# Performance work log

Measured on AMD Instinct MI355X. Metric: run time of the kernel, lower is better.

The kernel has to match this reference:

```python
import jax, jax.numpy as jnp
import numpy as np
import math

DIM = 1024
HEAD = 16


def setup_inputs() -> dict:
    key = jax.random.key(0)
    k1, k2, k3, k4, k5 = jax.random.split(key, 5)
    scale = 1.0 / math.sqrt(DIM)
    return {
        "x": jax.random.normal(k1, (2, 2048, DIM), dtype=jnp.float32),
        "W_kqv": jax.random.uniform(k2, (3 * DIM, DIM), minval=-scale, maxval=scale, dtype=jnp.float32),
        "b_kqv": jax.random.uniform(k3, (3 * DIM,), minval=-scale, maxval=scale, dtype=jnp.float32),
        "W_out": jax.random.uniform(k4, (DIM, DIM), minval=-scale, maxval=scale, dtype=jnp.float32),
        "b_out": jax.random.uniform(k5, (DIM,), minval=-scale, maxval=scale, dtype=jnp.float32),
    }


def reference(x, W_kqv, b_kqv, W_out, b_out):
    b, s, h = x.shape
    head = HEAD
    d = h // head
    # fused QKV projection (torch Linear: x @ W.T + b)
    kqv = jnp.einsum("bsh,oh->bso", x, W_kqv) + b_kqv  # [b, s, 3h]
    q, k, v = jnp.split(kqv, 3, axis=-1)
    # [b, s, h] -> [b, head, s, d]
    q = q.reshape(b, s, head, d).transpose(0, 2, 1, 3)
    k = k.reshape(b, s, head, d).transpose(0, 2, 1, 3)
    v = v.reshape(b, s, head, d).transpose(0, 2, 1, 3)
    scores = jnp.einsum("bnqd,bnkd->bnqk", q, k) / jnp.sqrt(jnp.float32(d))
    attn = jax.nn.softmax(scores, axis=-1)
    ctx = jnp.einsum("bnqk,bnkd->bnqd", attn, v)  # [b, head, s, d]
    ctx = ctx.transpose(0, 2, 1, 3).reshape(b, s, h)
    return jnp.einsum("bsh,oh->bso", ctx, W_out) + b_out
```

## Files before the change

kernel.cpp:

```cpp
#include <hip/hip_runtime.h>
#include <hip/hip_bf16.h>

#define DIM   1024
#define NHEAD 16
#define HD    64
#define SEQ   2048
#define BATCH 2
#define QKV3  3072

using short8 = __attribute__((ext_vector_type(8))) short;
using f32x4  = __attribute__((ext_vector_type(4))) float;

__device__ inline short f2bf(float f) {
    union { float f; unsigned u; } x; x.f = f;
    const unsigned r = (x.u + 0x7FFFu + ((x.u >> 16) & 1u)) >> 16;
    return (short)r;
}
__device__ inline unsigned pkbf(float a, float b) {
    union { __hip_bfloat162 h; unsigned u; } cv;
    cv.h = __float22bfloat162_rn(make_float2(a, b));
    return cv.u;
}

__device__ __forceinline__ void g2l16(const void* gptr, void* ldsbase) {
    __builtin_amdgcn_global_load_lds(
        (const __attribute__((address_space(1))) unsigned int*)(unsigned long long)gptr,
        (__attribute__((address_space(3))) unsigned int*)(unsigned int)(unsigned long long)ldsbase,
        16, 0, 0);
}

__global__ __launch_bounds__(256)
void conv_bf16(const float* __restrict__ x, const float* __restrict__ wk,
               const float* __restrict__ wo,
               unsigned short* __restrict__ xb, unsigned short* __restrict__ wkb,
               unsigned short* __restrict__ wob)
{
    const int bid = blockIdx.x;
    const float* src; unsigned short* dst; size_t base;
    if (bid < 1024)      { src = x;  dst = xb;  base = (size_t)bid * 4096; }
    else if (bid < 1792) { src = wk; dst = wkb; base = (size_t)(bid - 1024) * 4096; }
    else                 { src = wo; dst = wob; base = (size_t)(bid - 1792) * 4096; }
    const size_t off = base + threadIdx.x * 16;
    const float4 f0 = *(const float4*)(src + off + 0);
    const float4 f1 = *(const float4*)(src + off + 4);
    const float4 f2 = *(const float4*)(src + off + 8);
    const float4 f3 = *(const float4*)(src + off + 12);
    uint4 o0, o1;
    o0.x = pkbf(f0.x, f0.y); o0.y = pkbf(f0.z, f0.w);
    o0.z = pkbf(f1.x, f1.y); o0.w = pkbf(f1.z, f1.w);
    o1.x = pkbf(f2.x, f2.y); o1.y = pkbf(f2.z, f2.w);
    o1.z = pkbf(f3.x, f3.y); o1.w = pkbf(f3.z, f3.w);
    *(uint4*)(dst + off + 0) = o0;
    *(uint4*)(dst + off + 8) = o1;
}

__global__ __launch_bounds__(256)
void gemm_qkv(const unsigned short* __restrict__ A, const unsigned short* __restrict__ B,
              const float* __restrict__ bias,
              unsigned short* __restrict__ qbf, unsigned short* __restrict__ kbf,
              unsigned short* __restrict__ vtbf)
{
    constexpr int BK = 32, NIT = DIM / BK;
    const int K = DIM;
    __shared__ short As[2][128 * BK];
    __shared__ short Bs[2][128 * BK];

    const int tid  = threadIdx.x;
    const int lane = tid & 63;
    const int wave = tid >> 6;
    const int quad = lane >> 4;
    const int ln   = lane & 15;
    const int wm   = (wave & 1) * 64;
    const int wn   = (wave >> 1) * 64;

    const int bid = blockIdx.x;
    const int xcd = bid & 7;
    const int t   = bid >> 3;
    const int m0  = (xcd * 4 + (t & 3)) * 128;
    const int n0  = (t >> 2) * 128;

    int srow[2], sg[2];
#pragma unroll
    for (int i = 0; i < 2; ++i) {
        const int c  = wave * 128 + i * 64 + lane;
        srow[i] = c >> 2;
        sg[i]   = (c & 3) ^ ((srow[i] >> 1) & 3);
    }

    f32x4 acc[4][4];
#pragma unroll
    for (int i = 0; i < 4; ++i)
#pragma unroll
        for (int j = 0; j < 4; ++j) acc[i][j] = (f32x4){0.f, 0.f, 0.f, 0.f};

#pragma unroll
    for (int i = 0; i < 2; ++i) {
        const int cb = wave * 128 + i * 64;
        g2l16(A + (size_t)(m0 + srow[i]) * K + sg[i] * 8, &As[0][cb * 8]);
        g2l16(B + (size_t)(n0 + srow[i]) * K + sg[i] * 8, &Bs[0][cb * 8]);
    }
    __syncthreads();

    for (int kt = 0; kt < NIT; ++kt) {
        const int p = kt & 1;
        if (kt + 1 < NIT) {
            const int kn = (kt + 1) * BK;
#pragma unroll
            for (int i = 0; i < 2; ++i) {
                const int cb = wave * 128 + i * 64;
                g2l16(A + (size_t)(m0 + srow[i]) * K + kn + sg[i] * 8, &As[1 - p][cb * 8]);
                g2l16(B + (size_t)(n0 + srow[i]) * K + kn + sg[i] * 8, &Bs[1 - p][cb * 8]);
            }
        }

        short8 a[4], b[4];
#pragma unroll
        for (int i = 0; i < 4; ++i) {
            const int row = wm + i * 16 + ln;
            const int ch  = quad ^ ((row >> 1) & 3);
            a[i] = *(const short8*)&As[p][row * BK + ch * 8];
        }
#pragma unroll
        for (int j = 0; j < 4; ++j) {
            const int row = wn + j * 16 + ln;
            const int ch  = quad ^ ((row >> 1) & 3);
            b[j] = *(const short8*)&Bs[p][row * BK + ch * 8];
        }
#pragma unroll
        for (int i = 0; i < 4; ++i)
#pragma unroll
            for (int j = 0; j < 4; ++j)
                acc[i][j] = __builtin_amdgcn_mfma_f32_16x16x32_bf16(
                    a[i], b[j], acc[i][j], 0, 0, 0);
        __syncthreads();
    }

#pragma unroll
    for (int j = 0; j < 4; ++j) {
        const int col = n0 + wn + j * 16 + ln;
        const int sel = col >> 10;
        const int c   = col & 1023;
        const int hh  = c >> 6;
        const int dd  = c & 63;
        const float bv = bias[col];
        if (sel < 2) {
            unsigned short* dst = (sel == 0) ? qbf : kbf;
            const float qs = (sel == 0) ? 0.18033688f : 1.0f;
#pragma unroll
            for (int i = 0; i < 4; ++i)
#pragma unroll
                for (int r2 = 0; r2 < 4; ++r2) {
                    const int row = m0 + wm + i * 16 + quad * 4 + r2;
                    const int bb = row >> 11, ss = row & 2047;
                    dst[((size_t)(bb * NHEAD + hh) * SEQ + ss) * HD + dd] =
                        (unsigned short)f2bf((acc[i][j][r2] + bv) * qs);
                }
        } else {
            const int row0 = m0 + wm + quad * 4;
            const int bb = row0 >> 11;
            const size_t vbase = ((size_t)(bb * NHEAD + hh) * HD + dd) * SEQ;
#pragma unroll
            for (int i = 0; i < 4; ++i) {
                const int ss0 = (row0 & 2047) + i * 16;
                uint2 pk;
                pk.x = pkbf(acc[i][j][0] + bv, acc[i][j][1] + bv);
                pk.y = pkbf(acc[i][j][2] + bv, acc[i][j][3] + bv);
                *(uint2*)&vtbf[vbase + ss0] = pk;
            }
        }
    }
}

__global__ __launch_bounds__(512)
void attn_flash_mfma(const unsigned short* __restrict__ qbf,
                     const unsigned short* __restrict__ kbf,
                     const unsigned short* __restrict__ vtbf,
                     unsigned short* __restrict__ ctxbf)
{
    __shared__ short Ks[2][2][64 * 64];
    __shared__ short Vt[2][2][64 * 64];

    const int tid  = threadIdx.x;
    const int lane = tid & 63;
    const int wave = tid >> 6;
    const int hf   = wave >> 2;
    const int w4   = wave & 3;
    const int quad = lane >> 4;
    const int ln   = lane & 15;

    const int bid = blockIdx.x;
    const int bh  = bid & 31;
    const int qt  = bid >> 5;
    const int q0  = qt * 128;
    const int b   = bh >> 4;
    const int h   = bh & 15;

    const size_t sbase = (size_t)bh * SEQ * HD;
    const size_t vbase = (size_t)bh * HD * SEQ;
    const int kv0 = hf * (SEQ / 2);

    const int tloc = tid & 255;
    int srw[2], scg[2];
#pragma unroll
    for (int it = 0; it < 2; ++it) {
        const int ch = tloc + it * 256;
        srw[it] = ch >> 3;
        scg[it] = (ch & 7) ^ (srw[it] & 7);
    }

    short8 qf[2][2];
#pragma unroll
    for (int sm = 0; sm < 2; ++sm)
#pragma unroll
        for (int kc = 0; kc < 2; ++kc)
            qf[sm][kc] = *(const short8*)&qbf[sbase +
                (size_t)(q0 + w4 * 32 + sm * 16 + ln) * HD + kc * 32 + quad * 8];

#pragma unroll
    for (int it = 0; it < 2; ++it) {
        const int cb = tloc + it * 256;
        g2l16(kbf + sbase + (size_t)(kv0 + srw[it]) * HD + scg[it] * 8,
              &Ks[0][hf][cb * 8]);
        g2l16(vtbf + vbase + (size_t)srw[it] * SEQ + kv0 + scg[it] * 8,
              &Vt[0][hf][cb * 8]);
    }
    __syncthreads();

    f32x4 O[2][4];
#pragma unroll
    for (int sm = 0; sm < 2; ++sm)
#pragma unroll
        for (int dj = 0; dj < 4; ++dj) O[sm][dj] = (f32x4){0.f, 0.f, 0.f, 0.f};
    f32x4 lacc[2];
    lacc[0] = (f32x4){0.f, 0.f, 0.f, 0.f};
    lacc[1] = (f32x4){0.f, 0.f, 0.f, 0.f};

    short8 vone;
#pragma unroll
    for (int t = 0; t < 8; ++t) vone[t] = (short)0x3F80;

    constexpr int NIT = (SEQ / 2) / 64;
    for (int kt = 0; kt < NIT; ++kt) {
        const int p = kt & 1;
        if (kt + 1 < NIT) {
            const int k0n = kv0 + (kt + 1) * 64;
#pragma unroll
            for (int it = 0; it < 2; ++it) {
                const int cb = tloc + it * 256;
                g2l16(kbf + sbase + (size_t)(k0n + srw[it]) * HD + scg[it] * 8,
                      &Ks[1 - p][hf][cb * 8]);
                g2l16(vtbf + vbase + (size_t)srw[it] * SEQ + k0n + scg[it] * 8,
                      &Vt[1 - p][hf][cb * 8]);
            }
        }

        f32x4 st[2][4];
        __builtin_amdgcn_s_setprio(1);
#pragma unroll
        for (int j = 0; j < 4; ++j) {
            const int row = j * 16 + ln;
            const int c0 = quad ^ (row & 7);
            const int c1 = (4 + quad) ^ (row & 7);
            const short8 kf0 = *(const short8*)&Ks[p][hf][row * 64 + c0 * 8];
            const short8 kf1 = *(const short8*)&Ks[p][hf][row * 64 + c1 * 8];
#pragma unroll
            for (int sm = 0; sm < 2; ++sm) {
                f32x4 tt = __builtin_amdgcn_mfma_f32_16x16x32_bf16(
                    kf0, qf[sm][0], (f32x4){0.f, 0.f, 0.f, 0.f}, 0, 0, 0);
                st[sm][j] = __builtin_amdgcn_mfma_f32_16x16x32_bf16(
                    kf1, qf[sm][1], tt, 0, 0, 0);
            }
        }
        __builtin_amdgcn_s_setprio(0);

        short8 pf[2][2];
#pragma unroll
        for (int sm = 0; sm < 2; ++sm) {
            unsigned lo[4], hi[4];
#pragma unroll
            for (int j = 0; j < 4; ++j) {
                const float e0 = __builtin_amdgcn_exp2f(st[sm][j][0]);
                const float e1 = __builtin_amdgcn_exp2f(st[sm][j][1]);
                const float e2 = __builtin_amdgcn_exp2f(st[sm][j][2]);
                const float e3 = __builtin_amdgcn_exp2f(st[sm][j][3]);
                lo[j] = pkbf(e0, e1);
                hi[j] = pkbf(e2, e3);
            }
#pragma unroll
            for (int kc = 0; kc < 2; ++kc) {
                auto sa = __builtin_amdgcn_permlane32_swap(lo[2 * kc], lo[2 * kc + 1], false, false);
                auto sb = __builtin_amdgcn_permlane32_swap(hi[2 * kc], hi[2 * kc + 1], false, false);
                auto ua = __builtin_amdgcn_permlane16_swap(sa[0], sa[1], false, false);
                auto ub = __builtin_amdgcn_permlane16_swap(sb[0], sb[1], false, false);
                union { unsigned u[4]; short8 s; } cv;
                cv.u[0] = ua[0];
                cv.u[1] = ub[0];
                cv.u[2] = ua[1];
                cv.u[3] = ub[1];
                pf[sm][kc] = cv.s;
            }
        }

        __builtin_amdgcn_s_setprio(1);
#pragma unroll
        for (int kc = 0; kc < 2; ++kc) {
            lacc[0] = __builtin_amdgcn_mfma_f32_16x16x32_bf16(pf[0][kc], vone, lacc[0], 0, 0, 0);
            lacc[1] = __builtin_amdgcn_mfma_f32_16x16x32_bf16(pf[1][kc], vone, lacc[1], 0, 0, 0);
#pragma unroll
            for (int dj = 0; dj < 4; ++dj) {
                const int row = dj * 16 + ln;
                const int cg  = (kc * 4 + quad) ^ (row & 7);
                const short8 vf = *(const short8*)&Vt[p][hf][row * 64 + cg * 8];
                O[0][dj] = __builtin_amdgcn_mfma_f32_16x16x32_bf16(pf[0][kc], vf, O[0][dj], 0, 0, 0);
                O[1][dj] = __builtin_amdgcn_mfma_f32_16x16x32_bf16(pf[1][kc], vf, O[1][dj], 0, 0, 0);
            }
        }
        __builtin_amdgcn_s_setprio(0);
        __syncthreads();
    }

    float* Of = (float*)&Ks[0][0][0];
    float* Lf = (float*)&Vt[0][0][0];
    if (hf == 0) {
#pragma unroll
        for (int sm = 0; sm < 2; ++sm) {
#pragma unroll
            for (int dj = 0; dj < 4; ++dj)
#pragma unroll
                for (int r2 = 0; r2 < 4; ++r2)
                    Of[(w4 * 32 + sm * 16 + quad * 4 + r2) * 64 + dj * 16 + ln] =
                        O[sm][dj][r2];
            if (ln == 0)
#pragma unroll
                for (int r2 = 0; r2 < 4; ++r2)
                    Lf[w4 * 32 + sm * 16 + quad * 4 + r2] = lacc[sm][r2];
        }
    }
    __syncthreads();
    if (hf == 1) {
#pragma unroll
        for (int sm = 0; sm < 2; ++sm)
#pragma unroll
            for (int r2 = 0; r2 < 4; ++r2) {
                const int rr = w4 * 32 + sm * 16 + quad * 4 + r2;
                const float inv = 1.0f / (lacc[sm][r2] + Lf[rr]);
                const int row = b * SEQ + q0 + rr;
#pragma unroll
                for (int dj = 0; dj < 4; ++dj) {
                    const float val = O[sm][dj][r2] + Of[rr * 64 + dj * 16 + ln];
                    ctxbf[(size_t)row * DIM + h * HD + dj * 16 + ln] =
                        (unsigned short)f2bf(val * inv);
                }
            }
    }
}

__global__ __launch_bounds__(256)
void gemm_out(const unsigned short* __restrict__ A, const unsigned short* __restrict__ B,
              const float* __restrict__ bias, float* __restrict__ C)
{
    constexpr int BK = 32, NIT = DIM / BK;
    const int K = DIM, N = DIM;
    __shared__ short As[2][128 * BK];
    __shared__ short Bs[2][64 * BK];

    const int tid  = threadIdx.x;
    const int lane = tid & 63;
    const int wave = tid >> 6;
    const int quad = lane >> 4;
    const int ln   = lane & 15;
    const int wm   = (wave & 1) * 64;
    const int wn   = (wave >> 1) * 32;

    const int bid = blockIdx.x;
    const int xcd = bid & 7;
    const int t   = bid >> 3;
    const int m0  = (xcd * 4 + (t & 3)) * 128;
    const int n0  = (t >> 2) * 64;

    int srow[2], sg[2];
#pragma unroll
    for (int i = 0; i < 2; ++i) {
        const int c  = wave * 128 + i * 64 + lane;
        srow[i] = c >> 2;
        sg[i]   = (c & 3) ^ ((srow[i] >> 1) & 3);
    }
    const int cB  = wave * 64 + lane;
    const int brow = cB >> 2;
    const int bg   = (cB & 3) ^ ((brow >> 1) & 3);

    f32x4 acc[4][2];
#pragma unroll
    for (int i = 0; i < 4; ++i)
#pragma unroll
        for (int j = 0; j < 2; ++j) acc[i][j] = (f32x4){0.f, 0.f, 0.f, 0.f};

#pragma unroll
    for (int i = 0; i < 2; ++i)
        g2l16(A + (size_t)(m0 + srow[i]) * K + sg[i] * 8,
              &As[0][(wave * 128 + i * 64) * 8]);
    g2l16(B + (size_t)(n0 + brow) * K + bg * 8, &Bs[0][(wave * 64) * 8]);
    __syncthreads();

    for (int kt = 0; kt < NIT; ++kt) {
        const int p = kt & 1;
        if (kt + 1 < NIT) {
            const int kn = (kt + 1) * BK;
#pragma unroll
            for (int i = 0; i < 2; ++i)
                g2l16(A + (size_t)(m0 + srow[i]) * K + kn + sg[i] * 8,
                      &As[1 - p][(wave * 128 + i * 64) * 8]);
            g2l16(B + (size_t)(n0 + brow) * K + kn + bg * 8, &Bs[1 - p][(wave * 64) * 8]);
        }

        short8 a[4], b[2];
#pragma unroll
        for (int i = 0; i < 4; ++i) {
            const int row = wm + i * 16 + ln;
            const int ch  = quad ^ ((row >> 1) & 3);
            a[i] = *(const short8*)&As[p][row * BK + ch * 8];
        }
#pragma unroll
        for (int j = 0; j < 2; ++j) {
            const int row = wn + j * 16 + ln;
            const int ch  = quad ^ ((row >> 1) & 3);
            b[j] = *(const short8*)&Bs[p][row * BK + ch * 8];
        }
#pragma unroll
        for (int i = 0; i < 4; ++i)
#pragma unroll
            for (int j = 0; j < 2; ++j)
                acc[i][j] = __builtin_amdgcn_mfma_f32_16x16x32_bf16(
                    a[i], b[j], acc[i][j], 0, 0, 0);
        __syncthreads();
    }

#pragma unroll
    for (int j = 0; j < 2; ++j) {
        const int col = n0 + wn + j * 16 + ln;
        const float bv = bias[col];
#pragma unroll
        for (int i = 0; i < 4; ++i)
#pragma unroll
            for (int r2 = 0; r2 < 4; ++r2) {
                const int row = m0 + wm + i * 16 + quad * 4 + r2;
                C[(size_t)row * N + col] = acc[i][j][r2] + bv;
            }
    }
}

extern "C" void kernel_launch(void* const* d_in, const int* in_sizes, int n_in,
                              void* d_out, int out_size, void* d_ws, size_t ws_size,
                              hipStream_t stream)
{
    const float* x     = (const float*)d_in[0];
    const float* W_kqv = (const float*)d_in[1];
    const float* b_kqv = (const float*)d_in[2];
    const float* W_out = (const float*)d_in[3];
    const float* b_out = (const float*)d_in[4];
    float* out = (float*)d_out;

    char* w = (char*)d_ws;
    unsigned short* qbf   = (unsigned short*)w;  w += (size_t)BATCH * NHEAD * SEQ * HD * 2;
    unsigned short* kbf   = (unsigned short*)w;  w += (size_t)BATCH * NHEAD * SEQ * HD * 2;
    unsigned short* vtbf  = (unsigned short*)w;  w += (size_t)BATCH * NHEAD * HD * SEQ * 2;
    unsigned short* ctxbf = (unsigned short*)w;  w += (size_t)BATCH * SEQ * DIM * 2;
    unsigned short* xb    = (unsigned short*)w;  w += (size_t)BATCH * SEQ * DIM * 2;
    unsigned short* wkb   = (unsigned short*)w;  w += (size_t)QKV3 * DIM * 2;
    unsigned short* wob   = (unsigned short*)w;

    dim3 blk(256);

    conv_bf16<<<dim3(2048), blk, 0, stream>>>(x, W_kqv, W_out, xb, wkb, wob);

    gemm_qkv<<<dim3(768), blk, 0, stream>>>(xb, wkb, b_kqv, qbf, kbf, vtbf);

    attn_flash_mfma<<<dim3(512), dim3(512), 0, stream>>>(qbf, kbf, vtbf, ctxbf);

    gemm_out<<<dim3(512), blk, 0, stream>>>(ctxbf, wob, b_out, out);
}
```

Measured before the change: 175.9 us.

## Triple-buffer GEMM LDS stages with one barrier per K-step

Both projection GEMMs (QKV and output) move from double to triple-buffered LDS. Prefetch runs two K-tiles ahead, and explicit vmcnt waits let the current tile's loads finish while the next tile's loads stay in flight. Each K iteration now has a single barrier instead of two, and the next prefetch is issued after the LDS reads complete so it overlaps the MFMAs. This uses more LDS, which may reduce occupancy, and it relies on hand-set waitcnt values matching the number of async loads each thread issues.

```diff
diff --git a/kernel.cpp b/kernel.cpp
--- a/kernel.cpp
+++ b/kernel.cpp
@@ -62,8 +62,8 @@
 {
     constexpr int BK = 32, NIT = DIM / BK;
     const int K = DIM;
-    __shared__ short As[2][128 * BK];
-    __shared__ short Bs[2][128 * BK];
+    __shared__ short As[3][128 * BK];
+    __shared__ short Bs[3][128 * BK];
 
     const int tid  = threadIdx.x;
     const int lane = tid & 63;
@@ -94,45 +94,59 @@
         for (int j = 0; j < 4; ++j) acc[i][j] = (f32x4){0.f, 0.f, 0.f, 0.f};
 
 #pragma unroll
-    for (int i = 0; i < 2; ++i) {
-        const int cb = wave * 128 + i * 64;
-        g2l16(A + (size_t)(m0 + srow[i]) * K + sg[i] * 8, &As[0][cb * 8]);
-        g2l16(B + (size_t)(n0 + srow[i]) * K + sg[i] * 8, &Bs[0][cb * 8]);
-    }
-    __syncthreads();
-
+    for (int t0 = 0; t0 < 2; ++t0) {
+        const int kn = t0 * BK;
+#pragma unroll
+        for (int i = 0; i < 2; ++i) {
+            const int cb = wave * 128 + i * 64;
+            g2l16(A + (size_t)(m0 + srow[i]) * K + kn + sg[i] * 8, &As[t0][cb * 8]);
+            g2l16(B + (size_t)(n0 + srow[i]) * K + kn + sg[i] * 8, &Bs[t0][cb * 8]);
+        }
+    }
+
+    int bufc = 0;
+    int bufn = 2;
     for (int kt = 0; kt < NIT; ++kt) {
-        const int p = kt & 1;
-        if (kt + 1 < NIT) {
-            const int kn = (kt + 1) * BK;
-#pragma unroll
-            for (int i = 0; i < 2; ++i) {
-                const int cb = wave * 128 + i * 64;
-                g2l16(A + (size_t)(m0 + srow[i]) * K + kn + sg[i] * 8, &As[1 - p][cb * 8]);
-                g2l16(B + (size_t)(n0 + srow[i]) * K + kn + sg[i] * 8, &Bs[1 - p][cb * 8]);
-            }
-        }
+        if (kt < NIT - 1) asm volatile("s_waitcnt vmcnt(4)" ::: "memory");
+        else              asm volatile("s_waitcnt vmcnt(0)" ::: "memory");
+        __builtin_amdgcn_s_barrier();
+        __builtin_amdgcn_sched_barrier(0);
 
         short8 a[4], b[4];
 #pragma unroll
         for (int i = 0; i < 4; ++i) {
             const int row = wm + i * 16 + ln;
             const int ch  = quad ^ ((row >> 1) & 3);
-            a[i] = *(const short8*)&As[p][row * BK + ch * 8];
+            a[i] = *(const short8*)&As[bufc][row * BK + ch * 8];
         }
 #pragma unroll
         for (int j = 0; j < 4; ++j) {
             const int row = wn + j * 16 + ln;
             const int ch  = quad ^ ((row >> 1) & 3);
-            b[j] = *(const short8*)&Bs[p][row * BK + ch * 8];
-        }
+            b[j] = *(const short8*)&Bs[bufc][row * BK + ch * 8];
+        }
+        asm volatile("s_waitcnt lgkmcnt(0)" ::: "memory");
+        __builtin_amdgcn_sched_barrier(0);
+
+        if (kt + 2 < NIT) {
+            const int kn = (kt + 2) * BK;
+#pragma unroll
+            for (int i = 0; i < 2; ++i) {
+                const int cb = wave * 128 + i * 64;
+                g2l16(A + (size_t)(m0 + srow[i]) * K + kn + sg[i] * 8, &As[bufn][cb * 8]);
+                g2l16(B + (size_t)(n0 + srow[i]) * K + kn + sg[i] * 8, &Bs[bufn][cb * 8]);
+            }
+        }
+
 #pragma unroll
         for (int i = 0; i < 4; ++i)
 #pragma unroll
             for (int j = 0; j < 4; ++j)
                 acc[i][j] = __builtin_amdgcn_mfma_f32_16x16x32_bf16(
                     a[i], b[j], acc[i][j], 0, 0, 0);
-        __syncthreads();
+
+        bufc = (bufc == 2) ? 0 : bufc + 1;
+        bufn = (bufn == 2) ? 0 : bufn + 1;
     }
 
 #pragma unroll
@@ -361,8 +375,8 @@
 {
     constexpr int BK = 32, NIT = DIM / BK;
     const int K = DIM, N = DIM;
-    __shared__ short As[2][128 * BK];
-    __shared__ short Bs[2][64 * BK];
+    __shared__ short As[3][128 * BK];
+    __shared__ short Bs[3][64 * BK];
 
     const int tid  = threadIdx.x;
     const int lane = tid & 63;
@@ -396,43 +410,57 @@
         for (int j = 0; j < 2; ++j) acc[i][j] = (f32x4){0.f, 0.f, 0.f, 0.f};
 
 #pragma unroll
-    for (int i = 0; i < 2; ++i)
-        g2l16(A + (size_t)(m0 + srow[i]) * K + sg[i] * 8,
-              &As[0][(wave * 128 + i * 64) * 8]);
-    g2l16(B + (size_t)(n0 + brow) * K + bg * 8, &Bs[0][(wave * 64) * 8]);
-    __syncthreads();
-
+    for (int t0 = 0; t0 < 2; ++t0) {
+        const int kn = t0 * BK;
+#pragma unroll
+        for (int i = 0; i < 2; ++i)
+            g2l16(A + (size_t)(m0 + srow[i]) * K + kn + sg[i] * 8,
+                  &As[t0][(wave * 128 + i * 64) * 8]);
+        g2l16(B + (size_t)(n0 + brow) * K + kn + bg * 8, &Bs[t0][(wave * 64) * 8]);
+    }
+
+    int bufc = 0;
+    int bufn = 2;
     for (int kt = 0; kt < NIT; ++kt) {
-        const int p = kt & 1;
-        if (kt + 1 < NIT) {
-            const int kn = (kt + 1) * BK;
-#pragma unroll
-            for (int i = 0; i < 2; ++i)
-                g2l16(A + (size_t)(m0 + srow[i]) * K + kn + sg[i] * 8,
-                      &As[1 - p][(wave * 128 + i * 64) * 8]);
-            g2l16(B + (size_t)(n0 + brow) * K + kn + bg * 8, &Bs[1 - p][(wave * 64) * 8]);
-        }
+        if (kt < NIT - 1) asm volatile("s_waitcnt vmcnt(3)" ::: "memory");
+        else              asm volatile("s_waitcnt vmcnt(0)" ::: "memory");
+        __builtin_amdgcn_s_barrier();
+        __builtin_amdgcn_sched_barrier(0);
 
         short8 a[4], b[2];
 #pragma unroll
         for (int i = 0; i < 4; ++i) {
             const int row = wm + i * 16 + ln;
             const int ch  = quad ^ ((row >> 1) & 3);
-            a[i] = *(const short8*)&As[p][row * BK + ch * 8];
+            a[i] = *(const short8*)&As[bufc][row * BK + ch * 8];
         }
 #pragma unroll
         for (int j = 0; j < 2; ++j) {
             const int row = wn + j * 16 + ln;
             const int ch  = quad ^ ((row >> 1) & 3);
-            b[j] = *(const short8*)&Bs[p][row * BK + ch * 8];
-        }
+            b[j] = *(const short8*)&Bs[bufc][row * BK + ch * 8];
+        }
+        asm volatile("s_waitcnt lgkmcnt(0)" ::: "memory");
+        __builtin_amdgcn_sched_barrier(0);
+
+        if (kt + 2 < NIT) {
+            const int kn = (kt + 2) * BK;
+#pragma unroll
+            for (int i = 0; i < 2; ++i)
+                g2l16(A + (size_t)(m0 + srow[i]) * K + kn + sg[i] * 8,
+                      &As[bufn][(wave * 128 + i * 64) * 8]);
+            g2l16(B + (size_t)(n0 + brow) * K + kn + bg * 8, &Bs[bufn][(wave * 64) * 8]);
+        }
+
 #pragma unroll
         for (int i = 0; i < 4; ++i)
 #pragma unroll
             for (int j = 0; j < 2; ++j)
                 acc[i][j] = __builtin_amdgcn_mfma_f32_16x16x32_bf16(
                     a[i], b[j], acc[i][j], 0, 0, 0);
-        __syncthreads();
+
+        bufc = (bufc == 2) ? 0 : bufc + 1;
+        bufn = (bufn == 2) ? 0 : bufn + 1;
     }
 
 #pragma unroll
```

Result: faster. 172.1 us, median of 2 (-2.2%).

## Fuse fp32-to-bf16 conversion into GEMM loads and drop the conversion kernel

Applied to the files above, without the earlier changes.

Removes the separate conversion kernel. The QKV and output GEMMs now load fp32 x and weights directly into registers, convert them to bf16, and write them into swizzled LDS. The async global-to-LDS copies are replaced by a register-staged pipeline that prefetches two stages ahead, with manual vmcnt/lgkmcnt waits and barriers. This saves a launch and the bf16 intermediate round trip through memory. In exchange, each GEMM reads twice as many bytes, weight conversion is repeated by every tile that reads the same data, and register pressure goes up.

```diff
diff --git a/kernel.cpp b/kernel.cpp
--- a/kernel.cpp
+++ b/kernel.cpp
@@ -30,32 +30,7 @@
 }
 
 __global__ __launch_bounds__(256)
-void conv_bf16(const float* __restrict__ x, const float* __restrict__ wk,
-               const float* __restrict__ wo,
-               unsigned short* __restrict__ xb, unsigned short* __restrict__ wkb,
-               unsigned short* __restrict__ wob)
-{
-    const int bid = blockIdx.x;
-    const float* src; unsigned short* dst; size_t base;
-    if (bid < 1024)      { src = x;  dst = xb;  base = (size_t)bid * 4096; }
-    else if (bid < 1792) { src = wk; dst = wkb; base = (size_t)(bid - 1024) * 4096; }
-    else                 { src = wo; dst = wob; base = (size_t)(bid - 1792) * 4096; }
-    const size_t off = base + threadIdx.x * 16;
-    const float4 f0 = *(const float4*)(src + off + 0);
-    const float4 f1 = *(const float4*)(src + off + 4);
-    const float4 f2 = *(const float4*)(src + off + 8);
-    const float4 f3 = *(const float4*)(src + off + 12);
-    uint4 o0, o1;
-    o0.x = pkbf(f0.x, f0.y); o0.y = pkbf(f0.z, f0.w);
-    o0.z = pkbf(f1.x, f1.y); o0.w = pkbf(f1.z, f1.w);
-    o1.x = pkbf(f2.x, f2.y); o1.y = pkbf(f2.z, f2.w);
-    o1.z = pkbf(f3.x, f3.y); o1.w = pkbf(f3.z, f3.w);
-    *(uint4*)(dst + off + 0) = o0;
-    *(uint4*)(dst + off + 8) = o1;
-}
-
-__global__ __launch_bounds__(256)
-void gemm_qkv(const unsigned short* __restrict__ A, const unsigned short* __restrict__ B,
+void gemm_qkv(const float* __restrict__ A, const float* __restrict__ B,
               const float* __restrict__ bias,
               unsigned short* __restrict__ qbf, unsigned short* __restrict__ kbf,
               unsigned short* __restrict__ vtbf)
@@ -93,47 +68,76 @@
 #pragma unroll
         for (int j = 0; j < 4; ++j) acc[i][j] = (f32x4){0.f, 0.f, 0.f, 0.f};
 
-#pragma unroll
-    for (int i = 0; i < 2; ++i) {
-        const int cb = wave * 128 + i * 64;
-        g2l16(A + (size_t)(m0 + srow[i]) * K + sg[i] * 8, &As[0][cb * 8]);
-        g2l16(B + (size_t)(n0 + srow[i]) * K + sg[i] * 8, &Bs[0][cb * 8]);
-    }
-    __syncthreads();
-
-    for (int kt = 0; kt < NIT; ++kt) {
-        const int p = kt & 1;
-        if (kt + 1 < NIT) {
-            const int kn = (kt + 1) * BK;
-#pragma unroll
-            for (int i = 0; i < 2; ++i) {
-                const int cb = wave * 128 + i * 64;
-                g2l16(A + (size_t)(m0 + srow[i]) * K + kn + sg[i] * 8, &As[1 - p][cb * 8]);
-                g2l16(B + (size_t)(n0 + srow[i]) * K + kn + sg[i] * 8, &Bs[1 - p][cb * 8]);
-            }
-        }
-
-        short8 a[4], b[4];
-#pragma unroll
-        for (int i = 0; i < 4; ++i) {
-            const int row = wm + i * 16 + ln;
-            const int ch  = quad ^ ((row >> 1) & 3);
-            a[i] = *(const short8*)&As[p][row * BK + ch * 8];
-        }
-#pragma unroll
-        for (int j = 0; j < 4; ++j) {
-            const int row = wn + j * 16 + ln;
-            const int ch  = quad ^ ((row >> 1) & 3);
-            b[j] = *(const short8*)&Bs[p][row * BK + ch * 8];
-        }
-#pragma unroll
-        for (int i = 0; i < 4; ++i)
-#pragma unroll
-            for (int j = 0; j < 4; ++j)
-                acc[i][j] = __builtin_amdgcn_mfma_f32_16x16x32_bf16(
-                    a[i], b[j], acc[i][j], 0, 0, 0);
-        __syncthreads();
-    }
+#define QKV_STAGE_LOAD(RA, RB, kt2) do {                                        \
+    const int kn_ = (kt2) * BK;                                                 \
+    _Pragma("unroll") for (int i = 0; i < 2; ++i) {                             \
+        const float* pa = A + (size_t)(m0 + srow[i]) * K + kn_ + sg[i] * 8;     \
+        RA[2*i+0] = *(const float4*)(pa + 0);                                   \
+        RA[2*i+1] = *(const float4*)(pa + 4);                                   \
+        const float* pb = B + (size_t)(n0 + srow[i]) * K + kn_ + sg[i] * 8;     \
+        RB[2*i+0] = *(const float4*)(pb + 0);                                   \
+        RB[2*i+1] = *(const float4*)(pb + 4);                                   \
+    }                                                                           \
+} while (0)
+
+#define QKV_STAGE_WRITE(RA, RB, buf) do {                                       \
+    _Pragma("unroll") for (int i = 0; i < 2; ++i) {                             \
+        uint4 oa, ob;                                                           \
+        oa.x = pkbf(RA[2*i+0].x, RA[2*i+0].y);                                  \
+        oa.y = pkbf(RA[2*i+0].z, RA[2*i+0].w);                                  \
+        oa.z = pkbf(RA[2*i+1].x, RA[2*i+1].y);                                  \
+        oa.w = pkbf(RA[2*i+1].z, RA[2*i+1].w);                                  \
+        *(uint4*)&As[buf][(wave * 128 + i * 64 + lane) * 8] = oa;               \
+        ob.x = pkbf(RB[2*i+0].x, RB[2*i+0].y);                                  \
+        ob.y = pkbf(RB[2*i+0].z, RB[2*i+0].w);                                  \
+        ob.z = pkbf(RB[2*i+1].x, RB[2*i+1].y);                                  \
+        ob.w = pkbf(RB[2*i+1].z, RB[2*i+1].w);                                  \
+        *(uint4*)&Bs[buf][(wave * 128 + i * 64 + lane) * 8] = ob;               \
+    }                                                                           \
+} while (0)
+
+#define QKV_ITER(kt, RLA, RLB, RWA, RWB, pbuf) do {                             \
+    if ((kt) + 2 < NIT) QKV_STAGE_LOAD(RLA, RLB, (kt) + 2);                     \
+    short8 a_[4], b_[4];                                                        \
+    _Pragma("unroll") for (int i = 0; i < 4; ++i) {                             \
+        const int row = wm + i * 16 + ln;                                       \
+        const int ch  = quad ^ ((row >> 1) & 3);                                \
+        a_[i] = *(const short8*)&As[pbuf][row * BK + ch * 8];                    \
+    }                                                                           \
+    _Pragma("unroll") for (int j = 0; j < 4; ++j) {                             \
+        const int row = wn + j * 16 + ln;                                       \
+        const int ch  = quad ^ ((row >> 1) & 3);                                \
+        b_[j] = *(const short8*)&Bs[pbuf][row * BK + ch * 8];                    \
+    }                                                                           \
+    if ((kt) + 1 < NIT) {                                                       \
+        if ((kt) + 2 < NIT) asm volatile("s_waitcnt vmcnt(8)" ::: "memory");    \
+        else                asm volatile("s_waitcnt vmcnt(0)" ::: "memory");    \
+        QKV_STAGE_WRITE(RWA, RWB, 1 - (pbuf));                                  \
+    }                                                                           \
+    asm volatile("s_waitcnt lgkmcnt(0)" ::: "memory");                          \
+    __builtin_amdgcn_sched_barrier(0);                                          \
+    _Pragma("unroll") for (int i = 0; i < 4; ++i)                               \
+        _Pragma("unroll") for (int j = 0; j < 4; ++j)                           \
+            acc[i][j] = __builtin_amdgcn_mfma_f32_16x16x32_bf16(                \
+                a_[i], b_[j], acc[i][j], 0, 0, 0);                              \
+    __builtin_amdgcn_s_barrier();                                               \
+} while (0)
+
+    float4 rA0[4], rB0[4], rA1[4], rB1[4];
+    QKV_STAGE_LOAD(rA0, rB0, 0);
+    QKV_STAGE_LOAD(rA1, rB1, 1);
+    asm volatile("s_waitcnt vmcnt(8)" ::: "memory");
+    QKV_STAGE_WRITE(rA0, rB0, 0);
+    asm volatile("s_waitcnt lgkmcnt(0)" ::: "memory");
+    __builtin_amdgcn_s_barrier();
+
+    for (int kt = 0; kt < NIT; kt += 2) {
+        QKV_ITER(kt,     rA0, rB0, rA1, rB1, 0);
+        QKV_ITER(kt + 1, rA1, rB1, rA0, rB0, 1);
+    }
+#undef QKV_STAGE_LOAD
+#undef QKV_STAGE_WRITE
+#undef QKV_ITER
 
 #pragma unroll
     for (int j = 0; j < 4; ++j) {
@@ -356,7 +360,7 @@
 }
 
 __global__ __launch_bounds__(256)
-void gemm_out(const unsigned short* __restrict__ A, const unsigned short* __restrict__ B,
+void gemm_out(const unsigned short* __restrict__ A, const float* __restrict__ B,
               const float* __restrict__ bias, float* __restrict__ C)
 {
     constexpr int BK = 32, NIT = DIM / BK;
@@ -395,45 +399,67 @@
 #pragma unroll
         for (int j = 0; j < 2; ++j) acc[i][j] = (f32x4){0.f, 0.f, 0.f, 0.f};
 
-#pragma unroll
-    for (int i = 0; i < 2; ++i)
-        g2l16(A + (size_t)(m0 + srow[i]) * K + sg[i] * 8,
-              &As[0][(wave * 128 + i * 64) * 8]);
-    g2l16(B + (size_t)(n0 + brow) * K + bg * 8, &Bs[0][(wave * 64) * 8]);
-    __syncthreads();
-
-    for (int kt = 0; kt < NIT; ++kt) {
-        const int p = kt & 1;
-        if (kt + 1 < NIT) {
-            const int kn = (kt + 1) * BK;
-#pragma unroll
-            for (int i = 0; i < 2; ++i)
-                g2l16(A + (size_t)(m0 + srow[i]) * K + kn + sg[i] * 8,
-                      &As[1 - p][(wave * 128 + i * 64) * 8]);
-            g2l16(B + (size_t)(n0 + brow) * K + kn + bg * 8, &Bs[1 - p][(wave * 64) * 8]);
-        }
-
-        short8 a[4], b[2];
-#pragma unroll
-        for (int i = 0; i < 4; ++i) {
-            const int row = wm + i * 16 + ln;
-            const int ch  = quad ^ ((row >> 1) & 3);
-            a[i] = *(const short8*)&As[p][row * BK + ch * 8];
-        }
-#pragma unroll
-        for (int j = 0; j < 2; ++j) {
-            const int row = wn + j * 16 + ln;
-            const int ch  = quad ^ ((row >> 1) & 3);
-            b[j] = *(const short8*)&Bs[p][row * BK + ch * 8];
-        }
-#pragma unroll
-        for (int i = 0; i < 4; ++i)
-#pragma unroll
-            for (int j = 0; j < 2; ++j)
-                acc[i][j] = __builtin_amdgcn_mfma_f32_16x16x32_bf16(
-                    a[i], b[j], acc[i][j], 0, 0, 0);
-        __syncthreads();
-    }
+#define OUT_STAGE_LOAD(RA, RB, kt2) do {                                        \
+    const int kn_ = (kt2) * BK;                                                 \
+    _Pragma("unroll") for (int i = 0; i < 2; ++i)                               \
+        RA[i] = *(const uint4*)(A + (size_t)(m0 + srow[i]) * K + kn_ + sg[i] * 8); \
+    const float* pb = B + (size_t)(n0 + brow) * K + kn_ + bg * 8;               \
+    RB[0] = *(const float4*)(pb + 0);                                           \
+    RB[1] = *(const float4*)(pb + 4);                                           \
+} while (0)
+
+#define OUT_STAGE_WRITE(RA, RB, buf) do {                                       \
+    _Pragma("unroll") for (int i = 0; i < 2; ++i)                               \
+        *(uint4*)&As[buf][(wave * 128 + i * 64 + lane) * 8] = RA[i];            \
+    uint4 ob;                                                                   \
+    ob.x = pkbf(RB[0].x, RB[0].y); ob.y = pkbf(RB[0].z, RB[0].w);               \
+    ob.z = pkbf(RB[1].x, RB[1].y); ob.w = pkbf(RB[1].z, RB[1].w);               \
+    *(uint4*)&Bs[buf][(wave * 64 + lane) * 8] = ob;                             \
+} while (0)
+
+#define OUT_ITER(kt, RLA, RLB, RWA, RWB, pbuf) do {                             \
+    if ((kt) + 2 < NIT) OUT_STAGE_LOAD(RLA, RLB, (kt) + 2);                     \
+    short8 a_[4], b_[2];                                                        \
+    _Pragma("unroll") for (int i = 0; i < 4; ++i) {                             \
+        const int row = wm + i * 16 + ln;                                       \
+        const int ch  = quad ^ ((row >> 1) & 3);                                \
+        a_[i] = *(const short8*)&As[pbuf][row * BK + ch * 8];                    \
+    }                                                                           \
+    _Pragma("unroll") for (int j = 0; j < 2; ++j) {                             \
+        const int row = wn + j * 16 + ln;                                       \
+        const int ch  = quad ^ ((row >> 1) & 3);                                \
+        b_[j] = *(const short8*)&Bs[pbuf][row * BK + ch * 8];                    \
+    }                                                                           \
+    if ((kt) + 1 < NIT) {                                                       \
+        if ((kt) + 2 < NIT) asm volatile("s_waitcnt vmcnt(4)" ::: "memory");    \
+        else                asm volatile("s_waitcnt vmcnt(0)" ::: "memory");    \
+        OUT_STAGE_WRITE(RWA, RWB, 1 - (pbuf));                                  \
+    }                                                                           \
+    asm volatile("s_waitcnt lgkmcnt(0)" ::: "memory");                          \
+    __builtin_amdgcn_sched_barrier(0);                                          \
+    _Pragma("unroll") for (int i = 0; i < 4; ++i)                               \
+        _Pragma("unroll") for (int j = 0; j < 2; ++j)                           \
+            acc[i][j] = __builtin_amdgcn_mfma_f32_16x16x32_bf16(                \
+                a_[i], b_[j], acc[i][j], 0, 0, 0);                              \
+    __builtin_amdgcn_s_barrier();                                               \
+} while (0)
+
+    uint4  rA0[2], rA1[2];
+    float4 rB0[2], rB1[2];
+    OUT_STAGE_LOAD(rA0, rB0, 0);
+    OUT_STAGE_LOAD(rA1, rB1, 1);
+    asm volatile("s_waitcnt vmcnt(4)" ::: "memory");
+    OUT_STAGE_WRITE(rA0, rB0, 0);
+    asm volatile("s_waitcnt lgkmcnt(0)" ::: "memory");
+    __builtin_amdgcn_s_barrier();
+
+    for (int kt = 0; kt < NIT; kt += 2) {
+        OUT_ITER(kt,     rA0, rB0, rA1, rB1, 0);
+        OUT_ITER(kt + 1, rA1, rB1, rA0, rB0, 1);
+    }
+#undef OUT_STAGE_LOAD
+#undef OUT_STAGE_WRITE
+#undef OUT_ITER
 
 #pragma unroll
     for (int j = 0; j < 2; ++j) {
@@ -464,18 +490,13 @@
     unsigned short* qbf   = (unsigned short*)w;  w += (size_t)BATCH * NHEAD * SEQ * HD * 2;
     unsigned short* kbf   = (unsigned short*)w;  w += (size_t)BATCH * NHEAD * SEQ * HD * 2;
     unsigned short* vtbf  = (unsigned short*)w;  w += (size_t)BATCH * NHEAD * HD * SEQ * 2;
-    unsigned short* ctxbf = (unsigned short*)w;  w += (size_t)BATCH * SEQ * DIM * 2;
-    unsigned short* xb    = (unsigned short*)w;  w += (size_t)BATCH * SEQ * DIM * 2;
-    unsigned short* wkb   = (unsigned short*)w;  w += (size_t)QKV3 * DIM * 2;
-    unsigned short* wob   = (unsigned short*)w;
+    unsigned short* ctxbf = (unsigned short*)w;
 
     dim3 blk(256);
 
-    conv_bf16<<<dim3(2048), blk, 0, stream>>>(x, W_kqv, W_out, xb, wkb, wob);
-
-    gemm_qkv<<<dim3(768), blk, 0, stream>>>(xb, wkb, b_kqv, qbf, kbf, vtbf);
+    gemm_qkv<<<dim3(768), blk, 0, stream>>>(x, W_kqv, b_kqv, qbf, kbf, vtbf);
 
     attn_flash_mfma<<<dim3(512), dim3(512), 0, stream>>>(qbf, kbf, vtbf, ctxbf);
 
-    gemm_out<<<dim3(512), blk, 0, stream>>>(ctxbf, wob, b_out, out);
-}
+    gemm_out<<<dim3(512), blk, 0, stream>>>(ctxbf, W_out, b_out, out);
+}
```

Result: slower. 224.6 us (+27.7%).
